# Optimization experiments

Measured on AMD Instinct MI355X. Metric: run time of the kernel, lower is better.

## Reference

```python
import jax, jax.numpy as jnp
import numpy as np

EMBED = 1024
HEADS = 16
HDIM = 64
FF = 4096
N, S = 2, 2048
EPS = 1e-5


def _ln(x, g, b):
    m = jnp.mean(x, axis=-1, keepdims=True)
    v = jnp.mean((x - m) ** 2, axis=-1, keepdims=True)
    return (x - m) / jnp.sqrt(v + EPS) * g + b


def setup_inputs() -> dict:
    key = jax.random.key(0)
    ks = jax.random.split(key, 12)
    sd = 0.02
    inp = {
        'x': jax.random.normal(ks[0], (N, S, EMBED), dtype=jnp.float32),
        'mask': jnp.ones((N, 1, S, S), dtype=jnp.int32),
        'Wq': jax.random.normal(ks[1], (EMBED, HEADS * HDIM), dtype=jnp.float32) * sd,
        'bq': jnp.zeros((HEADS * HDIM,), dtype=jnp.float32),
        'Wk': jax.random.normal(ks[2], (EMBED, HEADS * HDIM), dtype=jnp.float32) * sd,
        'bk': jnp.zeros((HEADS * HDIM,), dtype=jnp.float32),
        'Wv': jax.random.normal(ks[3], (EMBED, HEADS * HDIM), dtype=jnp.float32) * sd,
        'bv': jnp.zeros((HEADS * HDIM,), dtype=jnp.float32),
        'Wo': jax.random.normal(ks[4], (HEADS * HDIM, EMBED), dtype=jnp.float32) * sd,
        'bo': jnp.zeros((EMBED,), dtype=jnp.float32),
        'g1': jnp.ones((EMBED,), dtype=jnp.float32),
        'beta1': jnp.zeros((EMBED,), dtype=jnp.float32),
        'g2': jnp.ones((EMBED,), dtype=jnp.float32),
        'beta2': jnp.zeros((EMBED,), dtype=jnp.float32),
        'W1': jax.random.normal(ks[5], (EMBED, FF), dtype=jnp.float32) * sd,
        'b1': jnp.zeros((FF,), dtype=jnp.float32),
        'W2': jax.random.normal(ks[6], (FF, EMBED), dtype=jnp.float32) * sd,
        'b2': jnp.zeros((EMBED,), dtype=jnp.float32),
    }
    return inp


def reference(x, mask, Wq, bq, Wk, bk, Wv, bv, Wo, bo, g1, beta1, g2, beta2, W1, b1, W2, b2):
    n, q_len, _ = x.shape
    # QKV projections, split into heads: [n, s, h, d]
    Q = (x @ Wq + bq).reshape(n, q_len, HEADS, HDIM)
    K = (x @ Wk + bk).reshape(n, q_len, HEADS, HDIM)
    V = (x @ Wv + bv).reshape(n, q_len, HEADS, HDIM)
    scores = jnp.einsum('nqhd,nkhd->nhqk', Q, K)
    scores = jnp.where(mask == 0, -jnp.inf, scores)
    # NOTE: original torch code is `attention / embed_size ** 1 / 2`,
    # which parses as (scores / embed_size) / 2 — replicated faithfully.
    attn = jax.nn.softmax(scores / EMBED / 2.0, axis=-1)
    ctx = jnp.einsum('nhqk,nkhd->nqhd', attn, V).reshape(n, q_len, HEADS * HDIM)
    proj = ctx @ Wo + bo
    h = _ln(proj + x, g1, beta1)  # dropout is identity (eval / p=0)
    ff = jax.nn.relu(h @ W1 + b1) @ W2 + b2
    out = _ln(ff + h, g2, beta2)
    return out
```

## Files before the change

### kernel.cpp

```cpp
#include <hip/hip_runtime.h>
#include <hip/hip_bf16.h>
#include <cstdint>
#include <cstddef>

#define EMBED 1024
#define SLEN  2048
#define NB    2
#define HEADS 16
#define HDIM  64
#define FFDIM 4096
#define ROWS  (NB * SLEN)
#define LOG2E 1.4426950408889634f

typedef __attribute__((ext_vector_type(8))) __bf16 bf16x8;
typedef __attribute__((ext_vector_type(4))) __bf16 bf16x4;
typedef __attribute__((ext_vector_type(4))) float  f32x4;
typedef __attribute__((ext_vector_type(4))) _Float16 f16x4;

__device__ __forceinline__ void gload_lds16(const void* g, void* l) {
  __builtin_amdgcn_global_load_lds(
      (const __attribute__((address_space(1))) void*)g,
      (__attribute__((address_space(3))) void*)l, 16, 0, 0);
}

#define SCHED() __builtin_amdgcn_sched_barrier(0)
#define BAR()                              \
  do {                                     \
    __builtin_amdgcn_s_barrier();          \
    __builtin_amdgcn_sched_barrier(0);     \
  } while (0)
#define WAITVM(N)                                           \
  do {                                                      \
    asm volatile("s_waitcnt vmcnt(" #N ")" ::: "memory");   \
  } while (0)
#define WAITLGKM(N)                                         \
  do {                                                      \
    asm volatile("s_waitcnt lgkmcnt(" #N ")" ::: "memory"); \
  } while (0)

__global__ __launch_bounds__(256) void prologue_k(
    const float* __restrict__ x, const int* __restrict__ mask,
    const float* __restrict__ Wq, const float* __restrict__ Wk,
    const float* __restrict__ Wv, const float* __restrict__ Wo,
    const float* __restrict__ W1, const float* __restrict__ W2,
    __bf16* __restrict__ xb, int* __restrict__ flags,
    __bf16* __restrict__ Wqt, __bf16* __restrict__ Wkt, __bf16* __restrict__ Wvt,
    __bf16* __restrict__ Wot, __bf16* __restrict__ W1t, __bf16* __restrict__ W2t) {
  const int b = blockIdx.x;
  const int tid = threadIdx.x;
  if (b < 3072) {
    __shared__ float t[64][65];
    const float* src;
    __bf16* dst;
    int R, C, tile;
    if (b < 1024) {
      const int w = b >> 8;
      tile = b & 255; R = 1024; C = 1024;
      src = (w == 0) ? Wq : (w == 1) ? Wk : (w == 2) ? Wv : Wo;
      dst = (w == 0) ? Wqt : (w == 1) ? Wkt : (w == 2) ? Wvt : Wot;
    } else if (b < 2048) {
      tile = b - 1024; R = 1024; C = 4096; src = W1; dst = W1t;
    } else {
      tile = b - 2048; R = 4096; C = 1024; src = W2; dst = W2t;
    }
    const int ct = C >> 6;
    const int tr = (tile / ct) * 64, tc = (tile % ct) * 64;
    const int tx = tid & 63;
    const int ty = tid >> 6;
#pragma unroll
    for (int i = 0; i < 16; ++i) {
      int a = ty * 16 + i;
      t[a][tx] = src[(size_t)(tr + a) * C + tc + tx];
    }
    __syncthreads();
#pragma unroll
    for (int i = 0; i < 16; ++i) {
      int bb = ty * 16 + i;
      dst[(size_t)(tc + bb) * R + tr + tx] = (__bf16)t[tx][bb];
    }
  } else if (b < 4096) {
    const int base = (b - 3072) * 1024;
#pragma unroll
    for (int it = 0; it < 4; ++it) {
      const int i = base + it * 256 + tid;
      float4 v = ((const float4*)x)[i];
      bf16x4 o;
      o.x = (__bf16)v.x; o.y = (__bf16)v.y; o.z = (__bf16)v.z; o.w = (__bf16)v.w;
      ((bf16x4*)xb)[i] = o;
    }
  } else {
    const int mb = b - 4096;
    const int kt = mb & 31, qt = (mb >> 5) & 15, n = mb >> 9;
    const int* base = mask + ((size_t)n * SLEN + qt * 128) * SLEN + kt * 64;
    const int rw = tid >> 4;
    const int cg = tid & 15;
    int ok = 1;
#pragma unroll
    for (int i = 0; i < 8; ++i) {
      int4 v = ((const int4*)(base + (size_t)(rw + i * 16) * SLEN))[cg];
      ok &= (v.x != 0) & (v.y != 0) & (v.z != 0) & (v.w != 0);
    }
    __shared__ int red;
    if (tid == 0) red = 1;
    __syncthreads();
    if (!ok) red = 0;
    __syncthreads();
    if (tid == 0) flags[mb] = red;
  }
}

template <int MODE>
__global__ __launch_bounds__(512, 1) void gemm256(
    const __bf16* __restrict__ A, const __bf16* __restrict__ Bt,
    const float* __restrict__ bias, const float* __restrict__ bias2,
    const float* __restrict__ bias3,
    void* __restrict__ outp, void* __restrict__ outp2, void* __restrict__ outp3,
    int M, int N, int K, int Kc, float oscale) {
  __shared__ __align__(16) char smem[131072];
  const int tid = threadIdx.x;
  const int lane = tid & 63;
  const int ntile = N >> 8;
  const int mt = M >> 8;
  const int cpx = gridDim.x >> 3;
  int u = (blockIdx.x & 7) * cpx + (blockIdx.x >> 3);
  int kz = 0;
  if constexpr (MODE == 5) {
    const int tiles = mt * ntile;
    kz = u / tiles;
    u -= kz * tiles;
  }
  int bm, bn;
  {
    const int G = (ntile >= 4) ? 4 : ntile;
    const int gsz = mt * G;
    const int g = u / gsz;
    const int rem = u - g * gsz;
    bm = rem / G;
    bn = g * G + rem % G;
  }
  const int trow = bm << 8, tcol = bn << 8;

  const int r0 = tid & 255;
  const int c0 = tid >> 8;
  const __bf16* Ag = A + (size_t)(trow + r0) * K + (size_t)kz * Kc + c0 * 8;
  const __bf16* Bg = Bt + (size_t)(tcol + r0) * K + (size_t)kz * Kc + c0 * 8;

  auto stage = [&](int buf, int kt) {
    const __bf16* a0 = Ag + (size_t)kt * 32;
    const __bf16* b0 = Bg + (size_t)kt * 32;
    char* la = smem + buf * 32768 + tid * 16;
    char* lb = la + 16384;
    gload_lds16(a0, la);
    gload_lds16(a0 + 16, la + 8192);
    gload_lds16(b0, lb);
    gload_lds16(b0 + 16, lb + 8192);
  };

  const int wave = tid >> 6;
  const int wr = wave >> 2;
  const int wc = wave & 3;
  const int l16 = lane & 15;
  const int g4 = lane >> 4;

  f32x4 acc[8][4];
#pragma unroll
  for (int i = 0; i < 8; ++i)
#pragma unroll
    for (int j = 0; j < 4; ++j) acc[i][j] = (f32x4)0.0f;

  const int nk = Kc >> 5;
  stage(0, 0);
  stage(1, 1);
  stage(2, 2);
  WAITVM(8);
  BAR();
  for (int kt = 0; kt < nk; ++kt) {
    const int cur = kt & 3;
    const char* base = smem + cur * 32768;
    bf16x8 af[8], bfr[4];
#pragma unroll
    for (int i = 0; i < 4; ++i)
      af[i] = *(const bf16x8*)(base + g4 * 4096 + (wr * 128 + i * 16 + l16) * 16);
#pragma unroll
    for (int j = 0; j < 4; ++j)
      bfr[j] = *(const bf16x8*)(base + 16384 + g4 * 4096 + (wc * 64 + j * 16 + l16) * 16);
    SCHED();
#pragma unroll
    for (int i = 4; i < 8; ++i)
      af[i] = *(const bf16x8*)(base + g4 * 4096 + (wr * 128 + i * 16 + l16) * 16);
    if (kt + 3 < nk) stage((kt + 3) & 3, kt + 3);
    SCHED();
    WAITLGKM(4);
    SCHED();
    __builtin_amdgcn_s_setprio(1);
#pragma unroll
    for (int mi = 0; mi < 4; ++mi)
#pragma unroll
      for (int ni = 0; ni < 4; ++ni)
        acc[mi][ni] =
            __builtin_amdgcn_mfma_f32_16x16x32_bf16(af[mi], bfr[ni], acc[mi][ni], 0, 0, 0);
    __builtin_amdgcn_s_setprio(0);
    SCHED();
    WAITLGKM(0);
    SCHED();
    __builtin_amdgcn_s_setprio(1);
#pragma unroll
    for (int mi = 4; mi < 8; ++mi)
#pragma unroll
      for (int ni = 0; ni < 4; ++ni)
        acc[mi][ni] =
            __builtin_amdgcn_mfma_f32_16x16x32_bf16(af[mi], bfr[ni], acc[mi][ni], 0, 0, 0);
    __builtin_amdgcn_s_setprio(0);
    if (kt + 3 < nk) {
      WAITVM(8);
    } else if (kt + 3 == nk) {
      WAITVM(4);
    } else if (kt + 2 == nk) {
      WAITVM(0);
    }
    BAR();
  }

  if constexpr (MODE == 5) {
#pragma unroll
    for (int mi = 0; mi < 8; ++mi)
#pragma unroll
      for (int ni = 0; ni < 4; ++ni) {
        const int col = tcol + wc * 64 + ni * 16 + l16;
#pragma unroll
        for (int r = 0; r < 4; ++r) {
          const int row = trow + wr * 128 + mi * 16 + g4 * 4 + r;
          ((_Float16*)outp)[(size_t)kz * M * N + (size_t)row * N + col] =
              (_Float16)acc[mi][ni][r];
        }
      }
  } else {
    const int sel = (MODE == 4) ? (tcol >> 10) : 0;
    const float* bp = (MODE == 4) ? (sel == 0 ? bias : sel == 1 ? bias2 : bias3) : bias;
    const int cc0 = (MODE == 4) ? (tcol & 1023) : tcol;
    const int n = trow >> 11;
    if (MODE == 4 && sel == 2) {
      __bf16(*repT)[136] = (__bf16(*)[136])smem;
#pragma unroll
      for (int h = 0; h < 2; ++h) {
        __syncthreads();
        if (wr == h) {
#pragma unroll
          for (int mi = 0; mi < 8; ++mi)
#pragma unroll
            for (int ni = 0; ni < 4; ++ni) {
              const int cl = wc * 64 + ni * 16 + l16;
              const float bcol = bp[cc0 + cl];
#pragma unroll
              for (int r = 0; r < 4; ++r)
                repT[cl][mi * 16 + g4 * 4 + r] = (__bf16)(acc[mi][ni][r] + bcol);
            }
        }
        __syncthreads();
#pragma unroll
        for (int it = 0; it < 8; ++it) {
          const int cidx = it * 512 + tid;
          const int cl = cidx >> 4, seg = cidx & 15;
          const int col = cc0 + cl, hh = col >> 6, dd = col & 63;
          *(bf16x8*)((__bf16*)outp3 + ((size_t)((n * HEADS + hh) * HDIM) + dd) * SLEN +
                     (trow & 2047) + h * 128 + seg * 8) = *(const bf16x8*)&repT[cl][seg * 8];
        }
      }
    } else {
      __bf16(*rep)[264] = (__bf16(*)[264])smem;
#pragma unroll
      for (int h = 0; h < 2; ++h) {
        __syncthreads();
        if (wr == h) {
#pragma unroll
          for (int mi = 0; mi < 8; ++mi)
#pragma unroll
            for (int ni = 0; ni < 4; ++ni) {
              const int cl = wc * 64 + ni * 16 + l16;
              float bcol = bp[cc0 + cl];
#pragma unroll
              for (int r = 0; r < 4; ++r) {
                float v = acc[mi][ni][r] + bcol;
                if constexpr (MODE == 4) {
                  if (sel == 0) v *= oscale;
                } else {
                  v = fmaxf(v, 0.0f);
                }
                rep[mi * 16 + g4 * 4 + r][cl] = (__bf16)v;
              }
            }
        }
        __syncthreads();
        if constexpr (MODE == 3) {
#pragma unroll
          for (int it = 0; it < 8; ++it) {
            const int cidx = it * 512 + tid;
            const int rl = cidx >> 5, seg = cidx & 31;
            *(bf16x8*)((__bf16*)outp + (size_t)(trow + h * 128 + rl) * N + tcol + seg * 8) =
                *(const bf16x8*)&rep[rl][seg * 8];
          }
        } else {
          __bf16* dst = (sel == 0) ? (__bf16*)outp : (__bf16*)outp2;
#pragma unroll
          for (int it = 0; it < 8; ++it) {
            const int cidx = it * 512 + tid;
            const int rl = cidx >> 5, seg = cidx & 31;
            const int col = cc0 + seg * 8, hh = col >> 6, d = col & 63;
            const int s = (trow & 2047) + h * 128 + rl;
            *(bf16x8*)(dst + ((size_t)((n * HEADS + hh) * SLEN) + s) * HDIM + d) =
                *(const bf16x8*)&rep[rl][seg * 8];
          }
        }
      }
    }
  }
}

__global__ __launch_bounds__(256, 2) void gemm_bt5(
    const __bf16* __restrict__ A, const __bf16* __restrict__ Bt,
    _Float16* __restrict__ outp, int M, int N, int K, int Kc) {
  __shared__ __align__(16) char smem[65536];
  const int tid = threadIdx.x;
  const int lane = tid & 63;
  const int ntile = N >> 7;
  const int cpx = gridDim.x >> 3;
  int u = (blockIdx.x & 7) * cpx + (blockIdx.x >> 3);
  const int tiles = (M >> 7) * ntile;
  const int kz = u / tiles;
  u -= kz * tiles;
  const int bm = u / ntile;
  const int bn = u % ntile;
  const int trow = bm << 7;
  const int tcol = bn << 7;

  const int c0 = tid >> 7;
  const int r0 = tid & 127;
  const __bf16* Ag = A + (size_t)(trow + r0) * K + (size_t)kz * Kc + c0 * 8;
  const __bf16* Bg = Bt + (size_t)(tcol + r0) * K + (size_t)kz * Kc + c0 * 8;

  auto stage = [&](int buf, int kt) {
    const __bf16* a0 = Ag + (size_t)kt * 32;
    const __bf16* b0 = Bg + (size_t)kt * 32;
    char* la = smem + buf * 16384 + tid * 16;
    char* lb = la + 8192;
    gload_lds16(a0, la);
    gload_lds16(a0 + 16, la + 4096);
    gload_lds16(b0, lb);
    gload_lds16(b0 + 16, lb + 4096);
  };

  const int wave = tid >> 6;
  const int wr = (wave >> 1) * 64;
  const int wc = (wave & 1) * 64;
  const int l16 = lane & 15;
  const int g4 = lane >> 4;

  f32x4 acc[4][4];
#pragma unroll
  for (int i = 0; i < 4; ++i)
#pragma unroll
    for (int j = 0; j < 4; ++j) acc[i][j] = (f32x4)0.0f;

  const int nk = Kc >> 5;
  stage(0, 0);
  stage(1, 1);
  stage(2, 2);
  WAITVM(8);
  BAR();
  for (int kt = 0; kt < nk; ++kt) {
    const int cur = kt & 3;
    const char* base = smem + cur * 16384;
    bf16x8 af[4], bfr[4];
#pragma unroll
    for (int i = 0; i < 4; ++i) {
      af[i]  = *(const bf16x8*)(base + g4 * 2048 + (wr + i * 16 + l16) * 16);
      bfr[i] = *(const bf16x8*)(base + 8192 + g4 * 2048 + (wc + i * 16 + l16) * 16);
    }
    if (kt + 3 < nk) stage((kt + 3) & 3, kt + 3);
    SCHED();
    WAITLGKM(0);
    SCHED();
    __builtin_amdgcn_s_setprio(1);
#pragma unroll
    for (int mi = 0; mi < 4; ++mi)
#pragma unroll
      for (int ni = 0; ni < 4; ++ni)
        acc[mi][ni] =
            __builtin_amdgcn_mfma_f32_16x16x32_bf16(af[mi], bfr[ni], acc[mi][ni], 0, 0, 0);
    __builtin_amdgcn_s_setprio(0);
    if (kt + 3 < nk) {
      WAITVM(8);
    } else if (kt + 3 == nk) {
      WAITVM(4);
    } else if (kt + 2 == nk) {
      WAITVM(0);
    }
    BAR();
  }
#pragma unroll
  for (int mi = 0; mi < 4; ++mi)
#pragma unroll
    for (int ni = 0; ni < 4; ++ni) {
      const int col = tcol + wc + ni * 16 + l16;
#pragma unroll
      for (int r = 0; r < 4; ++r) {
        const int row = trow + wr + mi * 16 + g4 * 4 + r;
        outp[(size_t)kz * M * N + (size_t)row * N + col] = (_Float16)acc[mi][ni][r];
      }
    }
}

__global__ __launch_bounds__(512, 2) void attn_k(const __bf16* __restrict__ Q,
                                                 const __bf16* __restrict__ K,
                                                 const __bf16* __restrict__ Vt,
                                                 const int* __restrict__ mask,
                                                 const int* __restrict__ flags,
                                                 __bf16* __restrict__ ctx) {
  const int tid = threadIdx.x, lane = tid & 63, wave = tid >> 6;
  const int l16 = lane & 15, g4 = lane >> 4;
  const int bid = blockIdx.x;
  const int lb = (bid & 7) * 64 + (bid >> 3);
  const int qt = lb & 15, h = (lb >> 4) & 15, n = lb >> 8;
  const int q0 = qt * 128 + wave * 16;
  const __bf16* Qh = Q + (size_t)(n * HEADS + h) * SLEN * HDIM;
  const __bf16* Kh = K + (size_t)(n * HEADS + h) * SLEN * HDIM;
  const __bf16* Vh = Vt + (size_t)(n * HEADS + h) * HDIM * SLEN;
  const int* Mh = mask + (size_t)n * SLEN * SLEN;
  const int* Fh = flags + (n * 16 + qt) * 32;

  __shared__ __bf16 KV[2][2][8][64][8];
  __shared__ __align__(16) __bf16 P_lds[8][16][72];

  const int srow = tid & 63;
  const int schunk = tid >> 6;
  const __bf16* Kg = Kh + (size_t)srow * HDIM + schunk * 8;
  const __bf16* Vg = Vh + (size_t)srow * SLEN + schunk * 8;
  auto stage = [&](int buf, int kb) {
    char* lk = (char*)&KV[buf][0][0][0][0] + tid * 16;
    char* lv = (char*)&KV[buf][1][0][0][0] + tid * 16;
    gload_lds16(Kg + (size_t)kb * 64 * HDIM, lk);
    gload_lds16(Vg + kb * 64, lv);
  };

  const unsigned long long fbits = __ballot(Fh[lane & 31] != 0);

  bf16x8 qf[2];
#pragma unroll
  for (int kd = 0; kd < 2; ++kd)
    qf[kd] = *(const bf16x8*)(Qh + (size_t)(q0 + l16) * HDIM + kd * 32 + g4 * 8);

  float m_ = -INFINITY, lsum = 0.0f;
  f32x4 o[4];
#pragma unroll
  for (int ni = 0; ni < 4; ++ni) o[ni] = (f32x4)0.0f;

  const int nt = SLEN / 64;
  stage(0, 0);
  stage(1, 1);
  WAITVM(2);
  BAR();
  int cur = 0;
  for (int kt = 0; kt < nt; ++kt) {
    const int kbase = kt * 64;
    const bool full = (fbits >> kt) & 1ull;
    bf16x8 kf[4][2], vf[2][4];
#pragma unroll
    for (int ni = 0; ni < 4; ++ni) {
      kf[ni][0] = *(const bf16x8*)&KV[cur][0][g4][ni * 16 + l16][0];
      kf[ni][1] = *(const bf16x8*)&KV[cur][0][4 + g4][ni * 16 + l16][0];
    }
    SCHED();
#pragma unroll
    for (int kb = 0; kb < 2; ++kb)
#pragma unroll
      for (int ni = 0; ni < 4; ++ni)
        vf[kb][ni] = *(const bf16x8*)&KV[cur][1][kb * 4 + g4][ni * 16 + l16][0];
    SCHED();
    WAITLGKM(8);
    SCHED();
    f32x4 s[4];
#pragma unroll
    for (int ni = 0; ni < 4; ++ni) s[ni] = (f32x4)0.0f;
    __builtin_amdgcn_s_setprio(1);
#pragma unroll
    for (int ni = 0; ni < 4; ++ni) {
      s[ni] = __builtin_amdgcn_mfma_f32_16x16x32_bf16(kf[ni][0], qf[0], s[ni], 0, 0, 0);
      s[ni] = __builtin_amdgcn_mfma_f32_16x16x32_bf16(kf[ni][1], qf[1], s[ni], 0, 0, 0);
    }
    __builtin_amdgcn_s_setprio(0);
    if (!full) {
#pragma unroll
      for (int ni = 0; ni < 4; ++ni)
#pragma unroll
        for (int r = 0; r < 4; ++r) {
          const int mk = Mh[(size_t)(q0 + l16) * SLEN + kbase + ni * 16 + 4 * g4 + r];
          s[ni][r] = mk ? s[ni][r] : -INFINITY;
        }
    }
    float a = fmaxf(fmaxf(s[0][0], s[0][1]), fmaxf(s[0][2], s[0][3]));
    float b = fmaxf(fmaxf(s[1][0], s[1][1]), fmaxf(s[1][2], s[1][3]));
    float c = fmaxf(fmaxf(s[2][0], s[2][1]), fmaxf(s[2][2], s[2][3]));
    float d = fmaxf(fmaxf(s[3][0], s[3][1]), fmaxf(s[3][2], s[3][3]));
    const float pmax = fmaxf(fmaxf(a, b), fmaxf(c, d));
    if (!__all(pmax <= m_ + 8.0f)) {
      float pm2 = fmaxf(m_, pmax);
      pm2 = fmaxf(pm2, __shfl_xor(pm2, 16));
      pm2 = fmaxf(pm2, __shfl_xor(pm2, 32));
      const float al = __builtin_amdgcn_exp2f(m_ - pm2);
      m_ = pm2;
      lsum *= al;
#pragma unroll
      for (int r = 0; r < 4; ++r) {
        const float ao = __shfl(al, 4 * g4 + r);
#pragma unroll
        for (int ni = 0; ni < 4; ++ni) o[ni][r] *= ao;
      }
    }
    float ls = 0.0f;
#pragma unroll
    for (int ni = 0; ni < 4; ++ni) {
      bf16x4 pk;
#pragma unroll
      for (int r = 0; r < 4; ++r) {
        const float p = __builtin_amdgcn_exp2f(s[ni][r] - m_);
        ls += p;
        pk[r] = (__bf16)p;
      }
      *(bf16x4*)&P_lds[wave][l16][ni * 16 + 4 * g4] = pk;
    }
    lsum += ls;
    bf16x8 pa[2];
#pragma unroll
    for (int kb = 0; kb < 2; ++kb)
      pa[kb] = *(const bf16x8*)&P_lds[wave][l16][kb * 32 + 8 * g4];
    SCHED();
    WAITLGKM(0);
    SCHED();
    __builtin_amdgcn_s_setprio(1);
#pragma unroll
    for (int kb = 0; kb < 2; ++kb)
#pragma unroll
      for (int ni = 0; ni < 4; ++ni)
        o[ni] = __builtin_amdgcn_mfma_f32_16x16x32_bf16(pa[kb], vf[kb][ni], o[ni], 0, 0, 0);
    __builtin_amdgcn_s_setprio(0);
    WAITVM(0);
    BAR();
    if (kt + 2 < nt) stage(cur, kt + 2);
    cur ^= 1;
  }
  {
    float l = lsum;
    l += __shfl_xor(l, 16);
    l += __shfl_xor(l, 32);
    lsum = l;
  }
#pragma unroll
  for (int r = 0; r < 4; ++r) {
    const float inv = __builtin_amdgcn_rcpf(__shfl(lsum, 4 * g4 + r));
#pragma unroll
    for (int ni = 0; ni < 4; ++ni) {
      ctx[((size_t)(n * SLEN) + q0 + 4 * g4 + r) * EMBED + h * HDIM + ni * 16 + l16] =
          (__bf16)(o[ni][r] * inv);
    }
  }
}

__global__ __launch_bounds__(256) void ln_fused_k(const _Float16* __restrict__ p, int nz,
                                                  const float* __restrict__ bias,
                                                  const __bf16* __restrict__ resb,
                                                  const float* __restrict__ gw,
                                                  const float* __restrict__ bw,
                                                  float* __restrict__ of,
                                                  __bf16* __restrict__ ob) {
  const int tid = threadIdx.x;
  const size_t row = blockIdx.x;
  float4 bb = ((const float4*)bias)[tid];
  bf16x4 rr = ((const bf16x4*)(resb + row * EMBED))[tid];
  float4 v;
  v.x = bb.x + (float)rr[0];
  v.y = bb.y + (float)rr[1];
  v.z = bb.z + (float)rr[2];
  v.w = bb.w + (float)rr[3];
  for (int z = 0; z < nz; ++z) {
    f16x4 pz = ((const f16x4*)(p + (size_t)z * ROWS * EMBED + row * EMBED))[tid];
    v.x += (float)pz[0]; v.y += (float)pz[1]; v.z += (float)pz[2]; v.w += (float)pz[3];
  }
  float s = v.x + v.y + v.z + v.w;
  float sq = v.x * v.x + v.y * v.y + v.z * v.z + v.w * v.w;
#pragma unroll
  for (int off = 1; off < 64; off <<= 1) {
    s += __shfl_xor(s, off);
    sq += __shfl_xor(sq, off);
  }
  __shared__ float red[8];
  if ((tid & 63) == 0) { red[tid >> 6] = s; red[4 + (tid >> 6)] = sq; }
  __syncthreads();
  s = red[0] + red[1] + red[2] + red[3];
  sq = red[4] + red[5] + red[6] + red[7];
  const float mean = s * (1.0f / EMBED);
  const float var = sq * (1.0f / EMBED) - mean * mean;
  const float rstd = rsqrtf(var + 1e-5f);
  float4 gv = ((const float4*)gw)[tid];
  float4 bv2 = ((const float4*)bw)[tid];
  float4 ov;
  ov.x = (v.x - mean) * rstd * gv.x + bv2.x;
  ov.y = (v.y - mean) * rstd * gv.y + bv2.y;
  ov.z = (v.z - mean) * rstd * gv.z + bv2.z;
  ov.w = (v.w - mean) * rstd * gv.w + bv2.w;
  if (of) ((float4*)(of + row * EMBED))[tid] = ov;
  if (ob) {
    bf16x4 oh;
    oh.x = (__bf16)ov.x; oh.y = (__bf16)ov.y; oh.z = (__bf16)ov.z; oh.w = (__bf16)ov.w;
    ((bf16x4*)(ob + row * EMBED))[tid] = oh;
  }
}

extern "C" void kernel_launch(void* const* d_in, const int* in_sizes, int n_in,
                              void* d_out, int out_size, void* d_ws, size_t ws_size,
                              hipStream_t stream) {
  (void)in_sizes; (void)n_in; (void)out_size;
  const float* x   = (const float*)d_in[0];
  const int*  mask = (const int*)d_in[1];
  const float* Wq = (const float*)d_in[2];  const float* bq  = (const float*)d_in[3];
  const float* Wk = (const float*)d_in[4];  const float* bk  = (const float*)d_in[5];
  const float* Wv = (const float*)d_in[6];  const float* bv  = (const float*)d_in[7];
  const float* Wo = (const float*)d_in[8];  const float* bo  = (const float*)d_in[9];
  const float* g1 = (const float*)d_in[10]; const float* be1 = (const float*)d_in[11];
  const float* g2 = (const float*)d_in[12]; const float* be2 = (const float*)d_in[13];
  const float* W1 = (const float*)d_in[14]; const float* b1  = (const float*)d_in[15];
  const float* W2 = (const float*)d_in[16]; const float* b2  = (const float*)d_in[17];

  char* ws = (char*)d_ws;
  size_t off = 0;
  auto alloc = [&](size_t bytes) -> void* {
    void* p = ws + off;
    off += (bytes + 255) & ~(size_t)255;
    return p;
  };
  __bf16* xb   = (__bf16*)alloc((size_t)ROWS * EMBED * 2);
  __bf16* Wqt  = (__bf16*)alloc((size_t)EMBED * EMBED * 2);
  __bf16* Wkt  = (__bf16*)alloc((size_t)EMBED * EMBED * 2);
  __bf16* Wvt  = (__bf16*)alloc((size_t)EMBED * EMBED * 2);
  __bf16* Wot  = (__bf16*)alloc((size_t)EMBED * EMBED * 2);
  __bf16* W1t  = (__bf16*)alloc((size_t)EMBED * FFDIM * 2);
  __bf16* W2t  = (__bf16*)alloc((size_t)FFDIM * EMBED * 2);
  __bf16* Qb   = (__bf16*)alloc((size_t)ROWS * EMBED * 2);
  __bf16* Kb   = (__bf16*)alloc((size_t)ROWS * EMBED * 2);
  __bf16* Vtb  = (__bf16*)alloc((size_t)ROWS * EMBED * 2);
  __bf16* ctxb = (__bf16*)alloc((size_t)ROWS * EMBED * 2);
  __bf16* hb    = (__bf16*)alloc((size_t)ROWS * EMBED * 2);
  __bf16* a1    = (__bf16*)alloc((size_t)ROWS * FFDIM * 2);
  int*   mflags = (int*)alloc(NB * 16 * 32 * sizeof(int));

  const size_t pneed = (size_t)4 * ROWS * EMBED * sizeof(_Float16);
  int kspF2;
  _Float16* pF2;
  if (off + pneed <= ws_size) {
    pF2 = (_Float16*)alloc(pneed);
    kspF2 = 4;
  } else {
    pF2 = (_Float16*)Qb;
    kspF2 = 2;
  }
  _Float16* pWo = (_Float16*)a1;

  prologue_k<<<5120, 256, 0, stream>>>(x, mask, Wq, Wk, Wv, Wo, W1, W2,
                                       xb, mflags, Wqt, Wkt, Wvt, Wot, W1t, W2t);

  gemm256<4><<<(ROWS / 256) * (3 * EMBED / 256), 512, 0, stream>>>(
      xb, Wqt, bq, bk, bv, Qb, Kb, Vtb, ROWS, 3 * EMBED, EMBED, EMBED, LOG2E / 2048.0f);
  attn_k<<<NB * HEADS * (SLEN / 128), 512, 0, stream>>>(Qb, Kb, Vtb, mask, mflags, ctxb);
  gemm_bt5<<<(ROWS / 128) * (EMBED / 128) * 2, 256, 0, stream>>>(
      ctxb, Wot, pWo, ROWS, EMBED, EMBED, EMBED / 2);
  ln_fused_k<<<ROWS, 256, 0, stream>>>(pWo, 2, bo, xb, g1, be1, nullptr, hb);
  gemm256<3><<<(ROWS / 256) * (FFDIM / 256), 512, 0, stream>>>(
      hb, W1t, b1, nullptr, nullptr, a1, nullptr, nullptr, ROWS, FFDIM, EMBED, EMBED, 1.0f);
  gemm256<5><<<(ROWS / 256) * (EMBED / 256) * kspF2, 512, 0, stream>>>(
      a1, W2t, nullptr, nullptr, nullptr, pF2, nullptr, nullptr,
      ROWS, EMBED, FFDIM, FFDIM / kspF2, 1.0f);
  ln_fused_k<<<ROWS, 256, 0, stream>>>(pF2, kspF2, b2, hb, g2, be2, (float*)d_out, nullptr);
}
```

Before: 260.3 us.

## Use 1024-thread blocks with 64x64 per-wave tiles in gemm256

New measurement: 317.8 us. +22.1%, slower.

```diff
diff --git a/kernel.cpp b/kernel.cpp
--- a/kernel.cpp
+++ b/kernel.cpp
@@ -110,7 +110,7 @@
 }
 
 template <int MODE>
-__global__ __launch_bounds__(512, 1) void gemm256(
+__global__ __launch_bounds__(1024, 1) void gemm256(
     const __bf16* __restrict__ A, const __bf16* __restrict__ Bt,
     const float* __restrict__ bias, const float* __restrict__ bias2,
     const float* __restrict__ bias3,
@@ -146,14 +146,10 @@
   const __bf16* Bg = Bt + (size_t)(tcol + r0) * K + (size_t)kz * Kc + c0 * 8;
 
   auto stage = [&](int buf, int kt) {
-    const __bf16* a0 = Ag + (size_t)kt * 32;
-    const __bf16* b0 = Bg + (size_t)kt * 32;
     char* la = smem + buf * 32768 + tid * 16;
     char* lb = la + 16384;
-    gload_lds16(a0, la);
-    gload_lds16(a0 + 16, la + 8192);
-    gload_lds16(b0, lb);
-    gload_lds16(b0 + 16, lb + 8192);
+    gload_lds16(Ag + (size_t)kt * 32, la);
+    gload_lds16(Bg + (size_t)kt * 32, lb);
   };
 
   const int wave = tid >> 6;
@@ -162,9 +158,9 @@
   const int l16 = lane & 15;
   const int g4 = lane >> 4;
 
-  f32x4 acc[8][4];
-#pragma unroll
-  for (int i = 0; i < 8; ++i)
+  f32x4 acc[4][4];
+#pragma unroll
+  for (int i = 0; i < 4; ++i)
 #pragma unroll
     for (int j = 0; j < 4; ++j) acc[i][j] = (f32x4)0.0f;
 
@@ -172,49 +168,33 @@
   stage(0, 0);
   stage(1, 1);
   stage(2, 2);
-  WAITVM(8);
+  WAITVM(4);
   BAR();
   for (int kt = 0; kt < nk; ++kt) {
     const int cur = kt & 3;
     const char* base = smem + cur * 32768;
-    bf16x8 af[8], bfr[4];
-#pragma unroll
-    for (int i = 0; i < 4; ++i)
-      af[i] = *(const bf16x8*)(base + g4 * 4096 + (wr * 128 + i * 16 + l16) * 16);
-#pragma unroll
-    for (int j = 0; j < 4; ++j)
-      bfr[j] = *(const bf16x8*)(base + 16384 + g4 * 4096 + (wc * 64 + j * 16 + l16) * 16);
-    SCHED();
-#pragma unroll
-    for (int i = 4; i < 8; ++i)
-      af[i] = *(const bf16x8*)(base + g4 * 4096 + (wr * 128 + i * 16 + l16) * 16);
+    bf16x8 af[4], bfr[4];
+#pragma unroll
+    for (int i = 0; i < 4; ++i) {
+      af[i]  = *(const bf16x8*)(base + g4 * 4096 + (wr * 64 + i * 16 + l16) * 16);
+      bfr[i] = *(const bf16x8*)(base + 16384 + g4 * 4096 + (wc * 64 + i * 16 + l16) * 16);
+    }
     if (kt + 3 < nk) stage((kt + 3) & 3, kt + 3);
     SCHED();
-    WAITLGKM(4);
+    WAITLGKM(0);
     SCHED();
     __builtin_amdgcn_s_setprio(1);
 #pragma unroll
     for (int mi = 0; mi < 4; ++mi)
-#pragma unroll
-      for (int ni = 0; ni < 4; ++ni)
-        acc[mi][ni] =
-            __builtin_amdgcn_mfma_f32_16x16x32_bf16(af[mi], bfr[ni], acc[mi][ni], 0, 0, 0);
-    __builtin_amdgcn_s_setprio(0);
-    SCHED();
-    WAITLGKM(0);
-    SCHED();
-    __builtin_amdgcn_s_setprio(1);
-#pragma unroll
-    for (int mi = 4; mi < 8; ++mi)
 #pragma unroll
       for (int ni = 0; ni < 4; ++ni)
         acc[mi][ni] =
             __builtin_amdgcn_mfma_f32_16x16x32_bf16(af[mi], bfr[ni], acc[mi][ni], 0, 0, 0);
     __builtin_amdgcn_s_setprio(0);
     if (kt + 3 < nk) {
-      WAITVM(8);
+      WAITVM(4);
     } else if (kt + 3 == nk) {
-      WAITVM(4);
+      WAITVM(2);
     } else if (kt + 2 == nk) {
       WAITVM(0);
     }
@@ -223,13 +203,13 @@
 
   if constexpr (MODE == 5) {
 #pragma unroll
-    for (int mi = 0; mi < 8; ++mi)
+    for (int mi = 0; mi < 4; ++mi)
 #pragma unroll
       for (int ni = 0; ni < 4; ++ni) {
         const int col = tcol + wc * 64 + ni * 16 + l16;
 #pragma unroll
         for (int r = 0; r < 4; ++r) {
-          const int row = trow + wr * 128 + mi * 16 + g4 * 4 + r;
+          const int row = trow + wr * 64 + mi * 16 + g4 * 4 + r;
           ((_Float16*)outp)[(size_t)kz * M * N + (size_t)row * N + col] =
               (_Float16)acc[mi][ni][r];
         }
@@ -244,22 +224,23 @@
 #pragma unroll
       for (int h = 0; h < 2; ++h) {
         __syncthreads();
-        if (wr == h) {
-#pragma unroll
-          for (int mi = 0; mi < 8; ++mi)
+        if ((wr >> 1) == h) {
+          const int rbase = (wr & 1) * 64;
+#pragma unroll
+          for (int mi = 0; mi < 4; ++mi)
 #pragma unroll
             for (int ni = 0; ni < 4; ++ni) {
               const int cl = wc * 64 + ni * 16 + l16;
               const float bcol = bp[cc0 + cl];
 #pragma unroll
               for (int r = 0; r < 4; ++r)
-                repT[cl][mi * 16 + g4 * 4 + r] = (__bf16)(acc[mi][ni][r] + bcol);
+                repT[cl][rbase + mi * 16 + g4 * 4 + r] = (__bf16)(acc[mi][ni][r] + bcol);
             }
         }
         __syncthreads();
 #pragma unroll
-        for (int it = 0; it < 8; ++it) {
-          const int cidx = it * 512 + tid;
+        for (int it = 0; it < 4; ++it) {
+          const int cidx = it * 1024 + tid;
           const int cl = cidx >> 4, seg = cidx & 15;
           const int col = cc0 + cl, hh = col >> 6, dd = col & 63;
           *(bf16x8*)((__bf16*)outp3 + ((size_t)((n * HEADS + hh) * HDIM) + dd) * SLEN +
@@ -271,9 +252,10 @@
 #pragma unroll
       for (int h = 0; h < 2; ++h) {
         __syncthreads();
-        if (wr == h) {
-#pragma unroll
-          for (int mi = 0; mi < 8; ++mi)
+        if ((wr >> 1) == h) {
+          const int rbase = (wr & 1) * 64;
+#pragma unroll
+          for (int mi = 0; mi < 4; ++mi)
 #pragma unroll
             for (int ni = 0; ni < 4; ++ni) {
               const int cl = wc * 64 + ni * 16 + l16;
@@ -286,15 +268,15 @@
                 } else {
                   v = fmaxf(v, 0.0f);
                 }
-                rep[mi * 16 + g4 * 4 + r][cl] = (__bf16)v;
+                rep[rbase + mi * 16 + g4 * 4 + r][cl] = (__bf16)v;
               }
             }
         }
         __syncthreads();
         if constexpr (MODE == 3) {
 #pragma unroll
-          for (int it = 0; it < 8; ++it) {
-            const int cidx = it * 512 + tid;
+          for (int it = 0; it < 4; ++it) {
+            const int cidx = it * 1024 + tid;
             const int rl = cidx >> 5, seg = cidx & 31;
             *(bf16x8*)((__bf16*)outp + (size_t)(trow + h * 128 + rl) * N + tcol + seg * 8) =
                 *(const bf16x8*)&rep[rl][seg * 8];
@@ -302,8 +284,8 @@
         } else {
           __bf16* dst = (sel == 0) ? (__bf16*)outp : (__bf16*)outp2;
 #pragma unroll
-          for (int it = 0; it < 8; ++it) {
-            const int cidx = it * 512 + tid;
+          for (int it = 0; it < 4; ++it) {
+            const int cidx = it * 1024 + tid;
             const int rl = cidx >> 5, seg = cidx & 31;
             const int col = cc0 + seg * 8, hh = col >> 6, d = col & 63;
             const int s = (trow & 2047) + h * 128 + rl;
@@ -667,15 +649,15 @@
   prologue_k<<<5120, 256, 0, stream>>>(x, mask, Wq, Wk, Wv, Wo, W1, W2,
                                        xb, mflags, Wqt, Wkt, Wvt, Wot, W1t, W2t);
 
-  gemm256<4><<<(ROWS / 256) * (3 * EMBED / 256), 512, 0, stream>>>(
+  gemm256<4><<<(ROWS / 256) * (3 * EMBED / 256), 1024, 0, stream>>>(
       xb, Wqt, bq, bk, bv, Qb, Kb, Vtb, ROWS, 3 * EMBED, EMBED, EMBED, LOG2E / 2048.0f);
   attn_k<<<NB * HEADS * (SLEN / 128), 512, 0, stream>>>(Qb, Kb, Vtb, mask, mflags, ctxb);
   gemm_bt5<<<(ROWS / 128) * (EMBED / 128) * 2, 256, 0, stream>>>(
       ctxb, Wot, pWo, ROWS, EMBED, EMBED, EMBED / 2);
   ln_fused_k<<<ROWS, 256, 0, stream>>>(pWo, 2, bo, xb, g1, be1, nullptr, hb);
-  gemm256<3><<<(ROWS / 256) * (FFDIM / 256), 512, 0, stream>>>(
+  gemm256<3><<<(ROWS / 256) * (FFDIM / 256), 1024, 0, stream>>>(
       hb, W1t, b1, nullptr, nullptr, a1, nullptr, nullptr, ROWS, FFDIM, EMBED, EMBED, 1.0f);
-  gemm256<5><<<(ROWS / 256) * (EMBED / 256) * kspF2, 512, 0, stream>>>(
+  gemm256<5><<<(ROWS / 256) * (EMBED / 256) * kspF2, 1024, 0, stream>>>(
       a1, W2t, nullptr, nullptr, nullptr, pF2, nullptr, nullptr,
       ROWS, EMBED, FFDIM, FFDIM / kspF2, 1.0f);
   ln_fused_k<<<ROWS, 256, 0, stream>>>(pF2, kspF2, b2, hb, g2, be2, (float*)d_out, nullptr);
```
